# Optimization experiments

Measured on AMD Instinct MI355X. Metric: run time of the kernel, lower is better.

Reference implementation:

```python
import jax, jax.numpy as jnp
import numpy as np

B, C, L = 32, 64, 512
PATCH_LEN = 16
PATCH_NUM = L // PATCH_LEN
H = 512          # hidden_dim
FF = 512         # moe_d_ff == hidden_dim per __init__
E = 8            # num_experts
TOP_K = 2


def setup_inputs() -> dict:
    key = jax.random.key(0)
    ks = jax.random.split(key, 8)
    s = 0.02
    return {
        "x": jax.random.normal(ks[0], (B, C, L), dtype=jnp.float32),
        "Wp": jax.random.normal(ks[1], (H, PATCH_LEN), dtype=jnp.float32) * s,
        "bp": jnp.zeros((H,), dtype=jnp.float32),
        "Wg": jax.random.normal(ks[2], (E, H), dtype=jnp.float32) * s,
        "Wgate": jax.random.normal(ks[3], (E, FF, H), dtype=jnp.float32) * s,
        "Wup": jax.random.normal(ks[4], (E, FF, H), dtype=jnp.float32) * s,
        "Wdown": jax.random.normal(ks[5], (E, H, FF), dtype=jnp.float32) * s,
    }


def reference(x, Wp, bp, Wg, Wgate, Wup, Wdown):
    b, c, l = x.shape
    # patchify: [B, C, P, patch_len] -> project to hidden
    p = x.reshape(b, c, PATCH_NUM, PATCH_LEN)
    h = jnp.einsum("bcpl,dl->bcpd", p, Wp) + bp          # [B,C,P,H]
    tokens = h.reshape(-1, H)                               # [T,H]
    T = tokens.shape[0]

    # router: softmax in fp32, then top-k (norm_topk_prob=False)
    logits = tokens @ Wg.T                                   # [T,E]
    rw = jax.nn.softmax(logits.astype(jnp.float32), axis=-1)
    topw, topi = jax.lax.top_k(rw, TOP_K)                    # [T,K]

    # dense per-(token,expert) combine weight, equiv. to gather/scatter combine
    w = jnp.zeros((T, E), dtype=jnp.float32)
    w = w.at[jnp.arange(T)[:, None], topi].add(topw)         # [T,E]

    out = jnp.zeros((T, H), dtype=tokens.dtype)
    for e in range(E):  # fixed small expert loop
        g = jax.nn.silu(tokens @ Wgate[e].T)
        u = tokens @ Wup[e].T
        y = (g * u) @ Wdown[e].T                             # [T,H]
        out = out + (w[:, e:e + 1] * y.astype(jnp.float32)).astype(tokens.dtype)

    return out.reshape(b, c * PATCH_NUM, H)
```

## Files before the change

kernel.cpp:

```cpp
#include <hip/hip_runtime.h>
#include <hip/hip_bf16.h>
#include <cstdint>
#include <cstddef>

typedef __attribute__((ext_vector_type(8))) short short8;
typedef __attribute__((ext_vector_type(4))) float f32x4;

#define GLL16(g, l) __builtin_amdgcn_global_load_lds(                         \
    (const __attribute__((address_space(1))) void*)(g),                        \
    (__attribute__((address_space(3))) void*)(l), 16, 0, 0)

constexpr int kB = 32, kC = 64, kL = 512;
constexpr int kPL = 16, kPN = 32;
constexpr int kH = 512, kFF = 512, kE = 8;
constexpr int kT = kB * kC * kPN;
constexpr int kTilesPerSlot = 520;
constexpr int kMaxTiles = 2 * kTilesPerSlot;
constexpr int kMaxPairs = kMaxTiles * 128;

constexpr size_t OFF_TOK  = 0;
constexpr size_t OFF_GU   = OFF_TOK + (size_t)kT * kH * 2;
constexpr size_t OFF_TOPI = OFF_GU + (size_t)kMaxPairs * kFF * 2;
constexpr size_t OFF_TOPW = OFF_TOPI + (size_t)kT * 4;
constexpr size_t OFF_CCNT = OFF_TOPW + (size_t)kT * 8;
constexpr size_t OFF_COFF = OFF_CCNT + 256 * 16 * 4;
constexpr size_t OFF_EOFF = OFF_COFF + 256 * 16 * 4;
constexpr size_t OFF_TILE = OFF_EOFF + 256;
constexpr size_t OFF_PTOK = OFF_TILE + ((kMaxTiles * 4 + 255) & ~255ull);
constexpr size_t OFF_PW   = OFF_PTOK + (size_t)kMaxPairs * 4;
constexpr size_t OFF_DUMP = OFF_PW + (size_t)kMaxPairs * 4;
constexpr size_t OFF_BG   = OFF_DUMP + 128 * 512 * 4;
constexpr size_t OFF_BU   = OFF_BG + (size_t)kE * kFF * kH * 2;
constexpr size_t OFF_BD   = OFF_BU + (size_t)kE * kFF * kH * 2;
constexpr size_t OFF_WC   = OFF_BD + (size_t)kE * kH * kFF * 2;
constexpr size_t OFF_BC   = OFF_WC + 8 * 16 * 8;

__global__ __launch_bounds__(256) void k_conv3(const float* __restrict__ a,
                                               const float* __restrict__ b,
                                               const float* __restrict__ c,
                                               __hip_bfloat16* __restrict__ da,
                                               __hip_bfloat16* __restrict__ db,
                                               __hip_bfloat16* __restrict__ dc, int n) {
  for (int i = blockIdx.x * blockDim.x + threadIdx.x; i < 3 * n; i += gridDim.x * blockDim.x) {
    int reg = i / n, j = i - reg * n;
    const float* s = (reg == 0) ? a : (reg == 1) ? b : c;
    __hip_bfloat16* d = (reg == 0) ? da : (reg == 1) ? db : dc;
    d[j] = __float2bfloat16(s[j]);
  }
}

__global__ void k_wcomb(const float* __restrict__ Wg, const float* __restrict__ Wp,
                        const float* __restrict__ bp, double* __restrict__ wc,
                        double* __restrict__ bc) {
  int tid = threadIdx.x;
  int e = tid >> 4, l = tid & 15;
  double s = 0.0;
  for (int d = 0; d < kH; ++d) s += (double)Wg[e * kH + d] * (double)Wp[d * kPL + l];
  wc[e * kPL + l] = s;
  if (l == 0) {
    double b = 0.0;
    for (int d = 0; d < kH; ++d) b += (double)Wg[e * kH + d] * (double)bp[d];
    bc[e] = b;
  }
}

__global__ __launch_bounds__(256) void k_patch(const float* __restrict__ x,
                                               const float* __restrict__ Wp,
                                               const float* __restrict__ bp,
                                               __hip_bfloat16* __restrict__ tok) {
  __shared__ float sWp[512 * 17];
  __shared__ float sx[128];
  __shared__ float sbp[512];
  int bb = blockIdx.x;
  int bc = bb >> 2, pg = bb & 3;
  int tid = threadIdx.x;
  for (int i = tid; i < 512 * 16; i += 256) sWp[(i >> 4) * 17 + (i & 15)] = Wp[i];
  if (tid < 128) sx[tid] = x[(size_t)bc * 512 + pg * 128 + tid];
  for (int i = tid; i < 512; i += 256) sbp[i] = bp[i];
  __syncthreads();
  for (int tl = 0; tl < 8; ++tl) {
    int t = bc * kPN + pg * 8 + tl;
    const float* xp = &sx[tl * 16];
    for (int d = tid; d < 512; d += 256) {
      float s = sbp[d];
#pragma unroll
      for (int l = 0; l < 16; ++l) s += xp[l] * sWp[d * 17 + l];
      tok[(size_t)t * kH + d] = __float2bfloat16(s);
    }
  }
}

__global__ __launch_bounds__(256) void k_router(const float* __restrict__ x,
                                                const double* __restrict__ wc,
                                                const double* __restrict__ bc,
                                                int* __restrict__ topi,
                                                float* __restrict__ topw,
                                                int* __restrict__ chunkCnt) {
  int t = blockIdx.x * 256 + threadIdx.x;
  int bci = t >> 5, p = t & 31;
  const float* xp = &x[(size_t)bci * 512 + p * 16];
  double xl[16];
#pragma unroll
  for (int l = 0; l < 16; ++l) xl[l] = (double)xp[l];
  double lo[8];
  double m = -1e300;
#pragma unroll
  for (int e = 0; e < 8; ++e) {
    double s = bc[e];
#pragma unroll
    for (int l = 0; l < 16; ++l) s += xl[l] * wc[e * 16 + l];
    lo[e] = s;
    m = fmax(m, s);
  }
  double den = 0.0;
#pragma unroll
  for (int e = 0; e < 8; ++e) {
    lo[e] = exp(lo[e] - m);
    den += lo[e];
  }
  int i1 = 0;
  double v1 = lo[0];
#pragma unroll
  for (int e = 1; e < 8; ++e)
    if (lo[e] > v1) { v1 = lo[e]; i1 = e; }
  int i2 = -1;
  double v2 = -1.0;
#pragma unroll
  for (int e = 0; e < 8; ++e)
    if (e != i1 && lo[e] > v2) { v2 = lo[e]; i2 = e; }
  topi[t] = i1 | (i2 << 4);
  topw[2 * t] = (float)(v1 / den);
  topw[2 * t + 1] = (float)(v2 / den);

  __shared__ int wsum[16][4];
  int wave = threadIdx.x >> 6, lane = threadIdx.x & 63;
#pragma unroll
  for (int seg = 0; seg < 16; ++seg) {
    int e = seg & 7;
    bool sel = (seg < 8) ? (i1 == e) : (i2 == e);
    unsigned long long mm = __ballot(sel);
    if (lane == 0) wsum[seg][wave] = __popcll(mm);
  }
  __syncthreads();
  if (threadIdx.x < 16)
    chunkCnt[blockIdx.x * 16 + threadIdx.x] =
        wsum[threadIdx.x][0] + wsum[threadIdx.x][1] + wsum[threadIdx.x][2] + wsum[threadIdx.x][3];
}

__global__ __launch_bounds__(256) void k_scan(const int* __restrict__ chunkCnt,
                                              int* __restrict__ chunkOff,
                                              int* __restrict__ eoff,
                                              int* __restrict__ tileExpert,
                                              int* __restrict__ pairTok,
                                              float* __restrict__ pairW) {
  int tid = threadIdx.x;
  __shared__ int cnt[256 * 16];
  __shared__ int coff[256 * 16];
  for (int i = tid; i < 256 * 16; i += 256) cnt[i] = chunkCnt[i];
  __syncthreads();
  __shared__ int totals[16];
  __shared__ int base[16];
  __shared__ int padded[16];
  if (tid < 16) {
    int run = 0;
    for (int c = 0; c < 256; ++c) {
      coff[c * 16 + tid] = run;
      run += cnt[c * 16 + tid];
    }
    totals[tid] = run;
  }
  __syncthreads();
  for (int i = tid; i < 256 * 16; i += 256) chunkOff[i] = coff[i];
  if (tid == 0) {
    for (int s = 0; s < 2; ++s) {
      int b = s * kTilesPerSlot * 128;
      for (int e = 0; e < 8; ++e) {
        int seg = s * 8 + e;
        base[seg] = b;
        padded[seg] = (totals[seg] + 127) & ~127;
        b += padded[seg];
      }
    }
  }
  __syncthreads();
  if (tid < 16) eoff[tid] = base[tid];
  for (int tI = tid; tI < kMaxTiles; tI += 256) tileExpert[tI] = -1;
  __syncthreads();
  for (int seg = 0; seg < 16; ++seg) {
    int e = seg & 7;
    int tile0 = base[seg] >> 7, nt = padded[seg] >> 7;
    for (int tI = tid; tI < nt; tI += 256) tileExpert[tile0 + tI] = e;
    for (int p = base[seg] + totals[seg] + tid; p < base[seg] + padded[seg]; p += 256) {
      pairTok[p] = -1;
      pairW[p] = 0.f;
    }
  }
}

__global__ __launch_bounds__(256) void k_fill(const int* __restrict__ topi,
                                              const float* __restrict__ topw,
                                              const int* __restrict__ chunkOff,
                                              const int* __restrict__ eoff,
                                              int* __restrict__ pairTok,
                                              float* __restrict__ pairW) {
  int chunk = blockIdx.x;
  int t = chunk * 256 + threadIdx.x;
  int pk = topi[t];
  int i1 = pk & 15, i2 = (pk >> 4) & 15;
  float w1 = topw[2 * t], w2 = topw[2 * t + 1];
  int wave = threadIdx.x >> 6, lane = threadIdx.x & 63;
  __shared__ int wsum[16][4];
  int pre[16];
  bool sel[16];
#pragma unroll
  for (int seg = 0; seg < 16; ++seg) {
    int e = seg & 7;
    sel[seg] = (seg < 8) ? (i1 == e) : (i2 == e);
    unsigned long long mm = __ballot(sel[seg]);
    pre[seg] = __popcll(mm & ((1ull << lane) - 1));
    if (lane == 0) wsum[seg][wave] = __popcll(mm);
  }
  __syncthreads();
#pragma unroll
  for (int seg = 0; seg < 16; ++seg) {
    if (!sel[seg]) continue;
    int woff = 0;
    for (int w = 0; w < wave; ++w) woff += wsum[seg][w];
    int pos = eoff[seg] + chunkOff[chunk * 16 + seg] + woff + pre[seg];
    pairTok[pos] = t;
    pairW[pos] = (seg < 8) ? w1 : w2;
  }
}


__global__ __launch_bounds__(256, 2) void k_gateup_sp(const __hip_bfloat16* __restrict__ tok,
                                                      const __hip_bfloat16* __restrict__ Wg0,
                                                      const __hip_bfloat16* __restrict__ Wu0,
                                                      const int* __restrict__ pairTok,
                                                      const int* __restrict__ tileExpert,
                                                      __hip_bfloat16* __restrict__ GU) {
  const int e = tileExpert[blockIdx.x];
  if (e < 0) return;
  __shared__ __hip_bfloat16 As[2][128 * 32];
  __shared__ __hip_bfloat16 Bgs[2][128 * 32];
  __shared__ __hip_bfloat16 Bus[2][128 * 32];
  const int tid = threadIdx.x;
  const int wid = tid >> 6, lane = tid & 63;
  const int tileBase = blockIdx.x * 128, tileN = blockIdx.y * 128;
  const int wr = wid >> 1, wcol = wid & 1;
  const int r = lane & 15, kq = lane >> 4;

  f32x4 accg[4][4] = {};
  f32x4 accu[4][4] = {};

  const char* Ab = (const char*)tok;
  const char* Bgb = (const char*)(Wg0 + (size_t)e * kFF * kH);
  const char* Bub = (const char*)(Wu0 + (size_t)e * kFF * kH);
  const int off0 = wid * 1024 + lane * 16;
  const int row0 = off0 >> 6;
  const int col0 = ((((off0 >> 4) & 3) ^ ((row0 >> 1) & 3)) << 4);
  const int off1 = off0 + 4096;
  const int row1 = off1 >> 6;
  const int col1 = ((((off1 >> 4) & 3) ^ ((row1 >> 1) & 3)) << 4);
  int t0i = pairTok[tileBase + row0];
  int t1i = pairTok[tileBase + row1];
  const size_t t0 = (size_t)(t0i < 0 ? 0 : t0i);
  const size_t t1 = (size_t)(t1i < 0 ? 0 : t1i);

  auto STAGE = [&](int buf, int kt) {
    const int kb = kt * 64;
    char* as = (char*)As[buf];
    char* bgs = (char*)Bgs[buf];
    char* bus = (char*)Bus[buf];
    GLL16(Ab + t0 * 1024 + kb + col0, as + wid * 1024);
    GLL16(Ab + t1 * 1024 + kb + col1, as + 4096 + wid * 1024);
    GLL16(Bgb + (size_t)(tileN + row0) * 1024 + kb + col0, bgs + wid * 1024);
    GLL16(Bgb + (size_t)(tileN + row1) * 1024 + kb + col1, bgs + 4096 + wid * 1024);
    GLL16(Bub + (size_t)(tileN + row0) * 1024 + kb + col0, bus + wid * 1024);
    GLL16(Bub + (size_t)(tileN + row1) * 1024 + kb + col1, bus + 4096 + wid * 1024);
  };

  STAGE(0, 0);
  __syncthreads();

#pragma unroll 2
  for (int kt = 0; kt < 16; ++kt) {
    const int cur = kt & 1;
    if (kt < 15) STAGE(cur ^ 1, kt + 1);

    short8 a[4], bg[4], bu[4];
#pragma unroll
    for (int i = 0; i < 4; ++i) {
      int row = wr * 64 + i * 16 + r;
      int sc = (kq ^ ((row >> 1) & 3)) << 3;
      a[i] = *(const short8*)&As[cur][row * 32 + sc];
    }
#pragma unroll
    for (int j = 0; j < 4; ++j) {
      int row = wcol * 64 + j * 16 + r;
      int sc = (kq ^ ((row >> 1) & 3)) << 3;
      bg[j] = *(const short8*)&Bgs[cur][row * 32 + sc];
      bu[j] = *(const short8*)&Bus[cur][row * 32 + sc];
    }
#pragma unroll
    for (int i = 0; i < 4; ++i)
#pragma unroll
      for (int j = 0; j < 4; ++j) {
        accg[i][j] = __builtin_amdgcn_mfma_f32_16x16x32_bf16(a[i], bg[j], accg[i][j], 0, 0, 0);
        accu[i][j] = __builtin_amdgcn_mfma_f32_16x16x32_bf16(a[i], bu[j], accu[i][j], 0, 0, 0);
      }
    __syncthreads();
  }

#pragma unroll
  for (int i = 0; i < 4; ++i)
#pragma unroll
    for (int j = 0; j < 4; ++j)
#pragma unroll
      for (int q = 0; q < 4; ++q) {
        int row = tileBase + wr * 64 + i * 16 + kq * 4 + q;
        int col = tileN + wcol * 64 + j * 16 + r;
        float g = accg[i][j][q], u = accu[i][j][q];
        float val = g / (1.f + __expf(-g)) * u;
        GU[(size_t)row * kFF + col] = __float2bfloat16(val);
      }
}

__global__ __launch_bounds__(256, 2) void k_down_sp(const __hip_bfloat16* __restrict__ GU,
                                                    const __hip_bfloat16* __restrict__ Wd0,
                                                    const int* __restrict__ pairTok,
                                                    const float* __restrict__ pairW,
                                                    const int* __restrict__ tileExpert,
                                                    float* __restrict__ out,
                                                    float* __restrict__ dump,
                                                    int tileOff, int first) {
  const int tile = tileOff + blockIdx.x;
  const int e = tileExpert[tile];
  if (e < 0) return;
  __shared__ __hip_bfloat16 As[2][128 * 32];
  __shared__ __hip_bfloat16 Bs[2][128 * 32];
  const int tid = threadIdx.x;
  const int wid = tid >> 6, lane = tid & 63;
  const int tileBase = tile * 128, tileN = blockIdx.y * 128;
  const int wr = wid >> 1, wcol = wid & 1;
  const int r = lane & 15, kq = lane >> 4;

  f32x4 acc[4][4] = {};

  const char* Ab = (const char*)GU;
  const char* Bb = (const char*)(Wd0 + (size_t)e * kH * kFF);
  const int off0 = wid * 1024 + lane * 16;
  const int row0 = off0 >> 6;
  const int col0 = ((((off0 >> 4) & 3) ^ ((row0 >> 1) & 3)) << 4);
  const int off1 = off0 + 4096;
  const int row1 = off1 >> 6;
  const int col1 = ((((off1 >> 4) & 3) ^ ((row1 >> 1) & 3)) << 4);

  auto STAGE = [&](int buf, int kt) {
    const int kb = kt * 64;
    char* as = (char*)As[buf];
    char* bs = (char*)Bs[buf];
    GLL16(Ab + (size_t)(tileBase + row0) * 1024 + kb + col0, as + wid * 1024);
    GLL16(Ab + (size_t)(tileBase + row1) * 1024 + kb + col1, as + 4096 + wid * 1024);
    GLL16(Bb + (size_t)(tileN + row0) * 1024 + kb + col0, bs + wid * 1024);
    GLL16(Bb + (size_t)(tileN + row1) * 1024 + kb + col1, bs + 4096 + wid * 1024);
  };

  STAGE(0, 0);
  __syncthreads();

#pragma unroll 2
  for (int kt = 0; kt < 16; ++kt) {
    const int cur = kt & 1;
    if (kt < 15) STAGE(cur ^ 1, kt + 1);

    short8 a[4], b[4];
#pragma unroll
    for (int i = 0; i < 4; ++i) {
      int row = wr * 64 + i * 16 + r;
      int sc = (kq ^ ((row >> 1) & 3)) << 3;
      a[i] = *(const short8*)&As[cur][row * 32 + sc];
    }
#pragma unroll
    for (int j = 0; j < 4; ++j) {
      int row = wcol * 64 + j * 16 + r;
      int sc = (kq ^ ((row >> 1) & 3)) << 3;
      b[j] = *(const short8*)&Bs[cur][row * 32 + sc];
    }
#pragma unroll
    for (int i = 0; i < 4; ++i)
#pragma unroll
      for (int j = 0; j < 4; ++j)
        acc[i][j] = __builtin_amdgcn_mfma_f32_16x16x32_bf16(a[i], b[j], acc[i][j], 0, 0, 0);
    __syncthreads();
  }

#pragma unroll
  for (int i = 0; i < 4; ++i)
#pragma unroll
    for (int q = 0; q < 4; ++q) {
      int prow = tileBase + wr * 64 + i * 16 + kq * 4 + q;
      float wv = pairW[prow];
      int tk = pairTok[prow];
      int colBase = tileN + wcol * 64 + r;
      float* orow = (tk >= 0) ? out + (size_t)tk * kH + colBase
                              : dump + (size_t)(prow & 127) * kH + colBase;
#pragma unroll
      for (int j = 0; j < 4; ++j) {
        float val = acc[i][j][q] * wv;
        if (first) orow[j * 16] = val;
        else orow[j * 16] += val;
      }
    }
}

extern "C" void kernel_launch(void* const* d_in, const int* in_sizes, int n_in,
                              void* d_out, int out_size, void* d_ws, size_t ws_size,
                              hipStream_t stream) {
  const float* x = (const float*)d_in[0];
  const float* Wp = (const float*)d_in[1];
  const float* bp = (const float*)d_in[2];
  const float* Wg = (const float*)d_in[3];
  const float* Wgate = (const float*)d_in[4];
  const float* Wup = (const float*)d_in[5];
  const float* Wdown = (const float*)d_in[6];
  float* out = (float*)d_out;

  char* ws = (char*)d_ws;
  __hip_bfloat16* tok = (__hip_bfloat16*)(ws + OFF_TOK);
  __hip_bfloat16* gu = (__hip_bfloat16*)(ws + OFF_GU);
  int* topi = (int*)(ws + OFF_TOPI);
  float* topw = (float*)(ws + OFF_TOPW);
  int* chunkCnt = (int*)(ws + OFF_CCNT);
  int* chunkOff = (int*)(ws + OFF_COFF);
  int* eoff = (int*)(ws + OFF_EOFF);
  int* tileExpert = (int*)(ws + OFF_TILE);
  int* pairTok = (int*)(ws + OFF_PTOK);
  float* pairW = (float*)(ws + OFF_PW);
  float* dump = (float*)(ws + OFF_DUMP);
  __hip_bfloat16* bgw = (__hip_bfloat16*)(ws + OFF_BG);
  __hip_bfloat16* buw = (__hip_bfloat16*)(ws + OFF_BU);
  __hip_bfloat16* bdw = (__hip_bfloat16*)(ws + OFF_BD);
  double* wc = (double*)(ws + OFF_WC);
  double* bcv = (double*)(ws + OFF_BC);

  const int nw = kE * kFF * kH;
  k_conv3<<<3072, 256, 0, stream>>>(Wgate, Wup, Wdown, bgw, buw, bdw, nw);
  k_wcomb<<<1, 128, 0, stream>>>(Wg, Wp, bp, wc, bcv);
  k_patch<<<8192, 256, 0, stream>>>(x, Wp, bp, tok);
  k_router<<<256, 256, 0, stream>>>(x, wc, bcv, topi, topw, chunkCnt);
  k_scan<<<1, 256, 0, stream>>>(chunkCnt, chunkOff, eoff, tileExpert, pairTok, pairW);
  k_fill<<<256, 256, 0, stream>>>(topi, topw, chunkOff, eoff, pairTok, pairW);

  dim3 gg(kMaxTiles, 4);
  k_gateup_sp<<<gg, 256, 0, stream>>>(tok, bgw, buw, pairTok, tileExpert, gu);
  dim3 gd(kTilesPerSlot, 4);
  k_down_sp<<<gd, 256, 0, stream>>>(gu, bdw, pairTok, pairW, tileExpert, out, dump, 0, 1);
  k_down_sp<<<gd, 256, 0, stream>>>(gu, bdw, pairTok, pairW, tileExpert, out, dump,
                                    kTilesPerSlot, 0);
}
```

Before: 558.1 us.

## Remap MoE GEMM grids so N-tiles share row tiles, and use explicit vmcnt waits

The 2D grid (tile, N-block) becomes a 1D grid where the four N-blocks of one row tile are adjacent block indices. Consecutive blocks then share the same gathered token rows and expert weights in cache. The double-buffered K loop replaces __syncthreads with explicit s_waitcnt vmcnt counts plus raw s_barrier and a sched_barrier. This lets the prefetch for the next stage stay in flight while the current stage is consumed. The hand-counted vmcnt values must match the number of global_load_lds issues per stage, and unroll is reduced to 1.

After: 544.5 us. 2.4% less time.

```diff
diff --git a/kernel.cpp b/kernel.cpp
--- a/kernel.cpp
+++ b/kernel.cpp
@@ -239,14 +239,15 @@
                                                       const int* __restrict__ pairTok,
                                                       const int* __restrict__ tileExpert,
                                                       __hip_bfloat16* __restrict__ GU) {
-  const int e = tileExpert[blockIdx.x];
+  const int tileIdx = blockIdx.x >> 2;
+  const int e = tileExpert[tileIdx];
   if (e < 0) return;
   __shared__ __hip_bfloat16 As[2][128 * 32];
   __shared__ __hip_bfloat16 Bgs[2][128 * 32];
   __shared__ __hip_bfloat16 Bus[2][128 * 32];
   const int tid = threadIdx.x;
   const int wid = tid >> 6, lane = tid & 63;
-  const int tileBase = blockIdx.x * 128, tileN = blockIdx.y * 128;
+  const int tileBase = tileIdx * 128, tileN = (blockIdx.x & 3) * 128;
   const int wr = wid >> 1, wcol = wid & 1;
   const int r = lane & 15, kq = lane >> 4;
 
@@ -281,12 +282,18 @@
   };
 
   STAGE(0, 0);
-  __syncthreads();
-
-#pragma unroll 2
+
+#pragma unroll 1
   for (int kt = 0; kt < 16; ++kt) {
     const int cur = kt & 1;
-    if (kt < 15) STAGE(cur ^ 1, kt + 1);
+    if (kt < 15) {
+      STAGE(cur ^ 1, kt + 1);
+      asm volatile("s_waitcnt vmcnt(6)" ::: "memory");
+    } else {
+      asm volatile("s_waitcnt vmcnt(0)" ::: "memory");
+    }
+    __builtin_amdgcn_s_barrier();
+    __builtin_amdgcn_sched_barrier(0);
 
     short8 a[4], bg[4], bu[4];
 #pragma unroll
@@ -309,7 +316,7 @@
         accg[i][j] = __builtin_amdgcn_mfma_f32_16x16x32_bf16(a[i], bg[j], accg[i][j], 0, 0, 0);
         accu[i][j] = __builtin_amdgcn_mfma_f32_16x16x32_bf16(a[i], bu[j], accu[i][j], 0, 0, 0);
       }
-    __syncthreads();
+    __builtin_amdgcn_s_barrier();
   }
 
 #pragma unroll
@@ -334,14 +341,14 @@
                                                     float* __restrict__ out,
                                                     float* __restrict__ dump,
                                                     int tileOff, int first) {
-  const int tile = tileOff + blockIdx.x;
+  const int tile = tileOff + (blockIdx.x >> 2);
   const int e = tileExpert[tile];
   if (e < 0) return;
   __shared__ __hip_bfloat16 As[2][128 * 32];
   __shared__ __hip_bfloat16 Bs[2][128 * 32];
   const int tid = threadIdx.x;
   const int wid = tid >> 6, lane = tid & 63;
-  const int tileBase = tile * 128, tileN = blockIdx.y * 128;
+  const int tileBase = tile * 128, tileN = (blockIdx.x & 3) * 128;
   const int wr = wid >> 1, wcol = wid & 1;
   const int r = lane & 15, kq = lane >> 4;
 
@@ -367,12 +374,18 @@
   };
 
   STAGE(0, 0);
-  __syncthreads();
-
-#pragma unroll 2
+
+#pragma unroll 1
   for (int kt = 0; kt < 16; ++kt) {
     const int cur = kt & 1;
-    if (kt < 15) STAGE(cur ^ 1, kt + 1);
+    if (kt < 15) {
+      STAGE(cur ^ 1, kt + 1);
+      asm volatile("s_waitcnt vmcnt(4)" ::: "memory");
+    } else {
+      asm volatile("s_waitcnt vmcnt(0)" ::: "memory");
+    }
+    __builtin_amdgcn_s_barrier();
+    __builtin_amdgcn_sched_barrier(0);
 
     short8 a[4], b[4];
 #pragma unroll
@@ -392,7 +405,7 @@
 #pragma unroll
       for (int j = 0; j < 4; ++j)
         acc[i][j] = __builtin_amdgcn_mfma_f32_16x16x32_bf16(a[i], b[j], acc[i][j], 0, 0, 0);
-    __syncthreads();
+    __builtin_amdgcn_s_barrier();
   }
 
 #pragma unroll
@@ -452,10 +465,9 @@
   k_scan<<<1, 256, 0, stream>>>(chunkCnt, chunkOff, eoff, tileExpert, pairTok, pairW);
   k_fill<<<256, 256, 0, stream>>>(topi, topw, chunkOff, eoff, pairTok, pairW);
 
-  dim3 gg(kMaxTiles, 4);
-  k_gateup_sp<<<gg, 256, 0, stream>>>(tok, bgw, buw, pairTok, tileExpert, gu);
-  dim3 gd(kTilesPerSlot, 4);
-  k_down_sp<<<gd, 256, 0, stream>>>(gu, bdw, pairTok, pairW, tileExpert, out, dump, 0, 1);
-  k_down_sp<<<gd, 256, 0, stream>>>(gu, bdw, pairTok, pairW, tileExpert, out, dump,
-                                    kTilesPerSlot, 0);
-}
+  k_gateup_sp<<<kMaxTiles * 4, 256, 0, stream>>>(tok, bgw, buw, pairTok, tileExpert, gu);
+  k_down_sp<<<kTilesPerSlot * 4, 256, 0, stream>>>(gu, bdw, pairTok, pairW, tileExpert, out,
+                                                   dump, 0, 1);
+  k_down_sp<<<kTilesPerSlot * 4, 256, 0, stream>>>(gu, bdw, pairTok, pairW, tileExpert, out,
+                                                   dump, kTilesPerSlot, 0);
+}
```
